# Kernel optimization log

Hardware: AMD Instinct MI355X
Metric: run time of the kernel (lower is better)

## Reference

```python
import jax, jax.numpy as jnp
import numpy as np

IN_F = 256
OUT_F = 256
ALPHA = 0.2  # LeakyReLU negative slope
NEG_INF = -9e15


def setup_inputs() -> dict:
    key = jax.random.key(0)
    k_h, k_adj, k_w, k_a = jax.random.split(key, 4)
    N = 8192
    h = jax.random.normal(k_h, (N, IN_F), dtype=jnp.float32)
    adj = jax.random.randint(k_adj, (N, N), 0, 2, dtype=jnp.int32)
    # xavier_uniform with gain=1.414
    gain = 1.414
    limW = gain * np.sqrt(6.0 / (IN_F + OUT_F))
    W = jax.random.uniform(k_w, (IN_F, OUT_F), minval=-limW, maxval=limW, dtype=jnp.float32)
    lima = gain * np.sqrt(6.0 / (2 * OUT_F + 1))
    a = jax.random.uniform(k_a, (2 * OUT_F, 1), minval=-lima, maxval=lima, dtype=jnp.float32)
    return {"h": h, "adj": adj, "W": W, "a": a}


def reference(h, adj, W, a):
    # Wh: [N, F]
    Wh = h @ W
    # The original materializes [N, N, 2F] concat pairs; equivalently
    # e[i, j] = leakyrelu(Wh[i] . a[:F] + Wh[j] . a[F:])
    a1 = a[:OUT_F, 0]  # [F]
    a2 = a[OUT_F:, 0]  # [F]
    s1 = Wh @ a1       # [N]
    s2 = Wh @ a2       # [N]
    e = jax.nn.leaky_relu(s1[:, None] + s2[None, :], negative_slope=ALPHA)  # [N, N]
    att = jnp.where(adj > 0, e, NEG_INF)
    att = jax.nn.softmax(att, axis=1)
    # dropout p=0.0 (eval) -> identity
    h_prime = att @ Wh  # [N, F]
    return jax.nn.elu(h_prime)  # concat=True path
```

## Files before the change

kernel.cpp:

```cpp
#include <hip/hip_runtime.h>

#define NN 8192
#define FF 256
#define PST 136

typedef _Float16 h8 __attribute__((ext_vector_type(8)));
typedef _Float16 h4 __attribute__((ext_vector_type(4)));
typedef float    f4 __attribute__((ext_vector_type(4)));
typedef int      i4v __attribute__((ext_vector_type(4)));

__device__ __forceinline__ unsigned fenc(float x) {
  unsigned u = __float_as_uint(x);
  return (u & 0x80000000u) ? ~u : (u | 0x80000000u);
}
__device__ __forceinline__ float fdec(unsigned e) {
  unsigned u = (e & 0x80000000u) ? (e ^ 0x80000000u) : ~e;
  return __uint_as_float(u);
}

__device__ __forceinline__ void sync_lds() {
  __builtin_amdgcn_s_waitcnt(0xc07f);
  __builtin_amdgcn_s_barrier();
}

__global__ __launch_bounds__(256) void k_wh(
    const float* __restrict__ h, const float* __restrict__ W,
    const float* __restrict__ a, _Float16* __restrict__ wfrag,
    float* __restrict__ s1, _Float16* __restrict__ s2h,
    unsigned* __restrict__ s2maxe) {
  __shared__ float hs[16 * 256];
  __shared__ _Float16 whs[16 * 264];
  const int t = threadIdx.x;
  const int r0 = blockIdx.x * 16;
#pragma unroll
  for (int i = 0; i < 4; ++i) {
    int idx = i * 1024 + t * 4;
    *(f4*)&hs[idx] = *(const f4*)&h[(size_t)r0 * 256 + idx];
  }
  __syncthreads();
  const int lane = t & 63;
  const int wv = t >> 6;
  const int rg = wv * 4;
  const int c4 = lane * 4;
  float acc[4][4];
#pragma unroll
  for (int i = 0; i < 4; ++i)
#pragma unroll
    for (int k = 0; k < 4; ++k) acc[i][k] = 0.f;
  f4 w[8];
#pragma unroll
  for (int i = 0; i < 8; ++i) w[i] = *(const f4*)&W[i * 256 + c4];
  for (int f = 0; f < 256; f += 8) {
    f4 nw[8];
    if (f < 248) {
#pragma unroll
      for (int i = 0; i < 8; ++i) nw[i] = *(const f4*)&W[(f + 8 + i) * 256 + c4];
    }
#pragma unroll
    for (int i = 0; i < 4; ++i) {
      f4 h0 = *(const f4*)&hs[(rg + i) * 256 + f];
      f4 h1 = *(const f4*)&hs[(rg + i) * 256 + f + 4];
#pragma unroll
      for (int k = 0; k < 4; ++k)
        acc[i][k] += h0[0]*w[0][k] + h0[1]*w[1][k] + h0[2]*w[2][k] + h0[3]*w[3][k]
                   + h1[0]*w[4][k] + h1[1]*w[5][k] + h1[2]*w[6][k] + h1[3]*w[7][k];
    }
    if (f < 248) {
#pragma unroll
      for (int i = 0; i < 8; ++i) w[i] = nw[i];
    }
  }
  float a1v[4], a2v[4];
#pragma unroll
  for (int k = 0; k < 4; ++k) { a1v[k] = a[c4 + k]; a2v[k] = a[256 + c4 + k]; }
#pragma unroll
  for (int i = 0; i < 4; ++i) {
    h4 hh;
    float p1 = 0.f, p2 = 0.f;
#pragma unroll
    for (int k = 0; k < 4; ++k) {
      hh[k] = (_Float16)acc[i][k];
      p1 += acc[i][k] * a1v[k];
      p2 += acc[i][k] * a2v[k];
    }
    *(h4*)&whs[(rg + i) * 264 + c4] = hh;
#pragma unroll
    for (int off = 32; off; off >>= 1) {
      p1 += __shfl_xor(p1, off);
      p2 += __shfl_xor(p2, off);
    }
    if (lane == 0) {
      const int r = r0 + rg + i;
      s1[r] = p1;
      s2h[r] = (_Float16)p2;
      atomicMax(s2maxe, fenc(p2));
    }
  }
  __syncthreads();
  {
    const int kt = blockIdx.x >> 1;
    const int hb = blockIdx.x & 1;
    const int lp = hb * 32 + (t & 31);
    const int kb = ((t & 31) >> 4) * 8;
    const int m16e = t & 15;
#pragma unroll
    for (int p = 0; p < 2; ++p) {
      const int n = (t >> 5) + p * 8;
      h8 v;
#pragma unroll
      for (int j = 0; j < 8; ++j) v[j] = whs[(kb + j) * 264 + n * 16 + m16e];
      *(h8*)&wfrag[(((size_t)kt * 16 + n) << 9) + lp * 8] = v;
    }
  }
}

__global__ __launch_bounds__(512, 4) void k_gat(
    const int* __restrict__ adj, const _Float16* __restrict__ wfrag,
    const float* __restrict__ s1g, const _Float16* __restrict__ s2h,
    const unsigned* __restrict__ s2maxe,
    float* __restrict__ o0, float* __restrict__ o1,
    float* __restrict__ lbuf) {
  __shared__ _Float16 P[2][32 * PST];
  __shared__ _Float16 s2l[4096];
  const int t = threadIdx.x;
  const int lane = t & 63;
  const int w = t >> 6;
  const int q = lane >> 4;
  const int m16 = lane & 15;
  const int rt = (int)blockIdx.x >> 1;
  const int kh = (int)blockIdx.x & 1;
  const int r0 = rt * 32;

  ((h8*)s2l)[t] = ((const h8*)(s2h + kh * 4096))[t];

  const int srow = 4 * w + q;
  const float s2m = fdec(*s2maxe);
  const float s1r = s1g[r0 + srow];
  const float u0 = s1r + s2m;
  const float mi = fmaxf(u0, 0.2f * u0);
  const float s1mi = s1r - mi;

  f4 acc[2][2];
#pragma unroll
  for (int m = 0; m < 2; ++m)
#pragma unroll
    for (int n = 0; n < 2; ++n)
#pragma unroll
      for (int e = 0; e < 4; ++e) acc[m][n][e] = 0.f;
  float lsum = 0.f;

  const int* adjp = adj + (size_t)(r0 + srow) * NN + kh * 4096 + m16 * 8;
  __syncthreads();

  i4v c0 = *(const i4v*)(adjp);
  i4v c1 = *(const i4v*)(adjp + 4);

  for (int p = 0; p < 32; ++p) {
    const _Float16* wfb =
        wfrag + ((((size_t)(kh * 128 + p * 4)) * 16 + 2 * w) << 9) + lane * 8;
    h8 bb[8];
#pragma unroll
    for (int ks = 0; ks < 4; ++ks) {
      bb[2 * ks]     = *(const h8*)(wfb + ks * 8192);
      bb[2 * ks + 1] = *(const h8*)(wfb + ks * 8192 + 512);
    }
    i4v n0 = c0, n1 = c1;
    if (p < 31) {
      n0 = *(const i4v*)(adjp + (p + 1) * 128);
      n1 = *(const i4v*)(adjp + (p + 1) * 128 + 4);
    }
    const h8 s2c = *(const h8*)&s2l[p * 128 + m16 * 8];
    h8 pa;
#pragma unroll
    for (int j = 0; j < 8; ++j) {
      const float s2v = (float)s2c[j];
      const float u = s1r + s2v;
      const float arg = s1mi + s2v - 0.8f * fminf(u, 0.f);
      const int msk = (j < 4) ? c0[j] : c1[j - 4];
      const float pv = (msk > 0) ? __expf(arg) : 0.f;
      lsum += pv;
      pa[j] = (_Float16)pv;
    }
    _Float16* Pb = &P[p & 1][0];
    *(h8*)&Pb[srow * PST + m16 * 8] = pa;
    sync_lds();
#pragma unroll
    for (int ks = 0; ks < 4; ++ks) {
      const h8 A0 = *(const h8*)&Pb[m16 * PST + ks * 32 + q * 8];
      const h8 A1 = *(const h8*)&Pb[(16 + m16) * PST + ks * 32 + q * 8];
      acc[0][0] = __builtin_amdgcn_mfma_f32_16x16x32_f16(A0, bb[2*ks],   acc[0][0], 0, 0, 0);
      acc[0][1] = __builtin_amdgcn_mfma_f32_16x16x32_f16(A0, bb[2*ks+1], acc[0][1], 0, 0, 0);
      acc[1][0] = __builtin_amdgcn_mfma_f32_16x16x32_f16(A1, bb[2*ks],   acc[1][0], 0, 0, 0);
      acc[1][1] = __builtin_amdgcn_mfma_f32_16x16x32_f16(A1, bb[2*ks+1], acc[1][1], 0, 0, 0);
    }
    c0 = n0; c1 = n1;
  }

  lsum += __shfl_xor(lsum, 1);
  lsum += __shfl_xor(lsum, 2);
  lsum += __shfl_xor(lsum, 4);
  lsum += __shfl_xor(lsum, 8);
  if (m16 == 0) lbuf[kh * NN + r0 + srow] = lsum;

  float* ob = kh ? o1 : o0;
#pragma unroll
  for (int m = 0; m < 2; ++m)
#pragma unroll
    for (int n = 0; n < 2; ++n)
#pragma unroll
      for (int v = 0; v < 4; ++v)
        ob[(size_t)(r0 + m * 16 + q * 4 + v) * FF + w * 32 + n * 16 + m16] =
            acc[m][n][v];
}

__global__ __launch_bounds__(256) void k_fin(
    float* __restrict__ out, const float* __restrict__ o1,
    const float* __restrict__ lbuf) {
  const int t = threadIdx.x;
  const int row = blockIdx.x * 16 + (t >> 4);
  const int c0 = (t & 15) * 16;
  const float linv = 1.0f / (lbuf[row] + lbuf[NN + row]);
#pragma unroll
  for (int i = 0; i < 4; ++i) {
    f4 v0 = *(const f4*)&out[(size_t)row * FF + c0 + i * 4];
    f4 v1 = *(const f4*)&o1[(size_t)row * FF + c0 + i * 4];
    f4 o;
#pragma unroll
    for (int e = 0; e < 4; ++e) {
      float x = (v0[e] + v1[e]) * linv;
      o[e] = (x > 0.f) ? x : (__expf(x) - 1.f);
    }
    *(f4*)&out[(size_t)row * FF + c0 + i * 4] = o;
  }
}

extern "C" void kernel_launch(void* const* d_in, const int* in_sizes, int n_in,
                              void* d_out, int out_size, void* d_ws, size_t ws_size,
                              hipStream_t stream) {
  const float* h   = (const float*)d_in[0];
  const int*   adj = (const int*)d_in[1];
  const float* W   = (const float*)d_in[2];
  const float* a   = (const float*)d_in[3];
  float* out = (float*)d_out;

  char* ws = (char*)d_ws;
  _Float16* wfrag = (_Float16*)ws;
  float*    o1    = (float*)(ws + (4u << 20));
  float*    lbuf  = (float*)(ws + (12u << 20));
  unsigned* s2me  = (unsigned*)(ws + (12u << 20) + 65536);
  float*    s1    = (float*)(ws + (12u << 20) + 65600);
  _Float16* s2h   = (_Float16*)(ws + (12u << 20) + 65600 + 32768);

  hipMemsetAsync(s2me, 0, 4, stream);
  k_wh<<<512, 256, 0, stream>>>(h, W, a, wfrag, s1, s2h, s2me);
  k_gat<<<512, 512, 0, stream>>>(adj, wfrag, s1, s2h, s2me, out, o1, lbuf);
  k_fin<<<512, 256, 0, stream>>>(out, o1, lbuf);
}
```

Baseline: 502.7 us.

## Prefetch adjacency into bitmask upfront and double-buffer wfrag B fragments

```diff
diff --git a/kernel.cpp b/kernel.cpp
--- a/kernel.cpp
+++ b/kernel.cpp
@@ -140,6 +140,26 @@
   const float mi = fmaxf(u0, 0.2f * u0);
   const float s1mi = s1r - mi;
 
+  const int* adjp = adj + (size_t)(r0 + srow) * NN + kh * 4096 + m16 * 8;
+  unsigned bits[8] = {0, 0, 0, 0, 0, 0, 0, 0};
+  {
+    i4v buf[16];
+#pragma unroll
+    for (int i = 0; i < 16; ++i)
+      buf[i] = __builtin_nontemporal_load(
+          (const i4v*)(adjp + (i >> 1) * 128 + (i & 1) * 4));
+#pragma unroll
+    for (int i = 0; i < 64; ++i) {
+      const i4v v = buf[i & 15];
+      if (i + 16 < 64)
+        buf[i & 15] = __builtin_nontemporal_load(
+            (const i4v*)(adjp + ((i + 16) >> 1) * 128 + ((i + 16) & 1) * 4));
+      const unsigned nib = (unsigned)(v[0] > 0) | ((unsigned)(v[1] > 0) << 1) |
+                           ((unsigned)(v[2] > 0) << 2) | ((unsigned)(v[3] > 0) << 3);
+      bits[i >> 3] |= nib << ((((i >> 1) & 3) << 3) + ((i & 1) << 2));
+    }
+  }
+
   f4 acc[2][2];
 #pragma unroll
   for (int m = 0; m < 2; ++m)
@@ -149,26 +169,30 @@
       for (int e = 0; e < 4; ++e) acc[m][n][e] = 0.f;
   float lsum = 0.f;
 
-  const int* adjp = adj + (size_t)(r0 + srow) * NN + kh * 4096 + m16 * 8;
   __syncthreads();
 
-  i4v c0 = *(const i4v*)(adjp);
-  i4v c1 = *(const i4v*)(adjp + 4);
-
-  for (int p = 0; p < 32; ++p) {
+  h8 bb[2][8];
+  {
     const _Float16* wfb =
-        wfrag + ((((size_t)(kh * 128 + p * 4)) * 16 + 2 * w) << 9) + lane * 8;
-    h8 bb[8];
+        wfrag + ((((size_t)(kh * 128)) * 16 + 2 * w) << 9) + lane * 8;
 #pragma unroll
     for (int ks = 0; ks < 4; ++ks) {
-      bb[2 * ks]     = *(const h8*)(wfb + ks * 8192);
-      bb[2 * ks + 1] = *(const h8*)(wfb + ks * 8192 + 512);
-    }
-    i4v n0 = c0, n1 = c1;
+      bb[0][2 * ks]     = *(const h8*)(wfb + ks * 8192);
+      bb[0][2 * ks + 1] = *(const h8*)(wfb + ks * 8192 + 512);
+    }
+  }
+
+  auto period = [&](int p, h8 (&bcur)[8], h8 (&bnxt)[8]) {
     if (p < 31) {
-      n0 = *(const i4v*)(adjp + (p + 1) * 128);
-      n1 = *(const i4v*)(adjp + (p + 1) * 128 + 4);
-    }
+      const _Float16* wfn =
+          wfrag + ((((size_t)(kh * 128 + (p + 1) * 4)) * 16 + 2 * w) << 9) + lane * 8;
+#pragma unroll
+      for (int ks = 0; ks < 4; ++ks) {
+        bnxt[2 * ks]     = *(const h8*)(wfn + ks * 8192);
+        bnxt[2 * ks + 1] = *(const h8*)(wfn + ks * 8192 + 512);
+      }
+    }
+    const unsigned byte = (bits[p >> 2] >> ((p & 3) << 3)) & 0xffu;
     const h8 s2c = *(const h8*)&s2l[p * 128 + m16 * 8];
     h8 pa;
 #pragma unroll
@@ -176,8 +200,7 @@
       const float s2v = (float)s2c[j];
       const float u = s1r + s2v;
       const float arg = s1mi + s2v - 0.8f * fminf(u, 0.f);
-      const int msk = (j < 4) ? c0[j] : c1[j - 4];
-      const float pv = (msk > 0) ? __expf(arg) : 0.f;
+      const float pv = (byte & (1u << j)) ? __expf(arg) : 0.f;
       lsum += pv;
       pa[j] = (_Float16)pv;
     }
@@ -188,12 +211,16 @@
     for (int ks = 0; ks < 4; ++ks) {
       const h8 A0 = *(const h8*)&Pb[m16 * PST + ks * 32 + q * 8];
       const h8 A1 = *(const h8*)&Pb[(16 + m16) * PST + ks * 32 + q * 8];
-      acc[0][0] = __builtin_amdgcn_mfma_f32_16x16x32_f16(A0, bb[2*ks],   acc[0][0], 0, 0, 0);
-      acc[0][1] = __builtin_amdgcn_mfma_f32_16x16x32_f16(A0, bb[2*ks+1], acc[0][1], 0, 0, 0);
-      acc[1][0] = __builtin_amdgcn_mfma_f32_16x16x32_f16(A1, bb[2*ks],   acc[1][0], 0, 0, 0);
-      acc[1][1] = __builtin_amdgcn_mfma_f32_16x16x32_f16(A1, bb[2*ks+1], acc[1][1], 0, 0, 0);
-    }
-    c0 = n0; c1 = n1;
+      acc[0][0] = __builtin_amdgcn_mfma_f32_16x16x32_f16(A0, bcur[2*ks],   acc[0][0], 0, 0, 0);
+      acc[0][1] = __builtin_amdgcn_mfma_f32_16x16x32_f16(A0, bcur[2*ks+1], acc[0][1], 0, 0, 0);
+      acc[1][0] = __builtin_amdgcn_mfma_f32_16x16x32_f16(A1, bcur[2*ks],   acc[1][0], 0, 0, 0);
+      acc[1][1] = __builtin_amdgcn_mfma_f32_16x16x32_f16(A1, bcur[2*ks+1], acc[1][1], 0, 0, 0);
+    }
+  };
+
+  for (int pp = 0; pp < 16; ++pp) {
+    period(2 * pp,     bb[0], bb[1]);
+    period(2 * pp + 1, bb[1], bb[0]);
   }
 
   lsum += __shfl_xor(lsum, 1);
```

Measured after the change: 537.5 us. 6.9% more time.

## Enlarge GAT row tile to 128 rows and split columns four ways

Applied to the files above, without the earlier changes.

```diff
diff --git a/kernel.cpp b/kernel.cpp
--- a/kernel.cpp
+++ b/kernel.cpp
@@ -114,123 +114,142 @@
   }
 }
 
-__global__ __launch_bounds__(512, 4) void k_gat(
+__global__ __launch_bounds__(512, 2) void k_gat(
     const int* __restrict__ adj, const _Float16* __restrict__ wfrag,
     const float* __restrict__ s1g, const _Float16* __restrict__ s2h,
     const unsigned* __restrict__ s2maxe,
     float* __restrict__ o0, float* __restrict__ o1,
+    float* __restrict__ o2, float* __restrict__ o3,
     float* __restrict__ lbuf) {
-  __shared__ _Float16 P[2][32 * PST];
-  __shared__ _Float16 s2l[4096];
+  __shared__ _Float16 P[2][128 * PST];
+  __shared__ _Float16 s2l[2048];
   const int t = threadIdx.x;
   const int lane = t & 63;
   const int w = t >> 6;
   const int q = lane >> 4;
   const int m16 = lane & 15;
-  const int rt = (int)blockIdx.x >> 1;
-  const int kh = (int)blockIdx.x & 1;
-  const int r0 = rt * 32;
-
-  ((h8*)s2l)[t] = ((const h8*)(s2h + kh * 4096))[t];
-
-  const int srow = 4 * w + q;
+  const int rt = (int)blockIdx.x >> 2;
+  const int kq = (int)blockIdx.x & 3;
+  const int r0 = rt * 128;
+
+  if (t < 256) ((h8*)s2l)[t] = ((const h8*)(s2h + kq * 2048))[t];
+
+  const int rloc = w * 16 + m16;
   const float s2m = fdec(*s2maxe);
-  const float s1r = s1g[r0 + srow];
+  const float s1r = s1g[r0 + rloc];
   const float u0 = s1r + s2m;
   const float mi = fmaxf(u0, 0.2f * u0);
   const float s1mi = s1r - mi;
 
-  f4 acc[2][2];
-#pragma unroll
-  for (int m = 0; m < 2; ++m)
+  f4 acc[8][2];
+#pragma unroll
+  for (int mt = 0; mt < 8; ++mt)
 #pragma unroll
     for (int n = 0; n < 2; ++n)
 #pragma unroll
-      for (int e = 0; e < 4; ++e) acc[m][n][e] = 0.f;
+      for (int e = 0; e < 4; ++e) acc[mt][n][e] = 0.f;
   float lsum = 0.f;
 
-  const int* adjp = adj + (size_t)(r0 + srow) * NN + kh * 4096 + m16 * 8;
+  const int* adjp = adj + (size_t)(r0 + rloc) * NN + kq * 2048 + q * 8;
   __syncthreads();
 
-  i4v c0 = *(const i4v*)(adjp);
-  i4v c1 = *(const i4v*)(adjp + 4);
-
-  for (int p = 0; p < 32; ++p) {
-    const _Float16* wfb =
-        wfrag + ((((size_t)(kh * 128 + p * 4)) * 16 + 2 * w) << 9) + lane * 8;
+  i4v adjc[8], adjn[8];
+#pragma unroll
+  for (int ks = 0; ks < 4; ++ks) {
+    adjc[2 * ks]     = __builtin_nontemporal_load((const i4v*)(adjp + ks * 32));
+    adjc[2 * ks + 1] = __builtin_nontemporal_load((const i4v*)(adjp + ks * 32 + 4));
+  }
+
+  for (int p = 0; p < 16; ++p) {
+    const int kb = kq * 64 + p * 4;
     h8 bb[8];
 #pragma unroll
     for (int ks = 0; ks < 4; ++ks) {
-      bb[2 * ks]     = *(const h8*)(wfb + ks * 8192);
-      bb[2 * ks + 1] = *(const h8*)(wfb + ks * 8192 + 512);
-    }
-    i4v n0 = c0, n1 = c1;
-    if (p < 31) {
-      n0 = *(const i4v*)(adjp + (p + 1) * 128);
-      n1 = *(const i4v*)(adjp + (p + 1) * 128 + 4);
-    }
-    const h8 s2c = *(const h8*)&s2l[p * 128 + m16 * 8];
-    h8 pa;
-#pragma unroll
-    for (int j = 0; j < 8; ++j) {
-      const float s2v = (float)s2c[j];
-      const float u = s1r + s2v;
-      const float arg = s1mi + s2v - 0.8f * fminf(u, 0.f);
-      const int msk = (j < 4) ? c0[j] : c1[j - 4];
-      const float pv = (msk > 0) ? __expf(arg) : 0.f;
-      lsum += pv;
-      pa[j] = (_Float16)pv;
+      const _Float16* wfb =
+          wfrag + (((size_t)(kb + ks) * 16 + 2 * w) << 9) + lane * 8;
+      bb[2 * ks]     = *(const h8*)(wfb);
+      bb[2 * ks + 1] = *(const h8*)(wfb + 512);
+    }
+    if (p < 15) {
+#pragma unroll
+      for (int ks = 0; ks < 4; ++ks) {
+        adjn[2 * ks]     = __builtin_nontemporal_load(
+            (const i4v*)(adjp + (p + 1) * 128 + ks * 32));
+        adjn[2 * ks + 1] = __builtin_nontemporal_load(
+            (const i4v*)(adjp + (p + 1) * 128 + ks * 32 + 4));
+      }
     }
     _Float16* Pb = &P[p & 1][0];
-    *(h8*)&Pb[srow * PST + m16 * 8] = pa;
+#pragma unroll
+    for (int ks = 0; ks < 4; ++ks) {
+      const h8 s2c = *(const h8*)&s2l[p * 128 + ks * 32 + q * 8];
+      const i4v a0 = adjc[2 * ks];
+      const i4v a1 = adjc[2 * ks + 1];
+      h8 pa;
+#pragma unroll
+      for (int j = 0; j < 8; ++j) {
+        const float s2v = (float)s2c[j];
+        const float u = s1r + s2v;
+        const float arg = s1mi + s2v - 0.8f * fminf(u, 0.f);
+        const int msk = (j < 4) ? a0[j] : a1[j - 4];
+        const float pv = (msk > 0) ? __expf(arg) : 0.f;
+        lsum += pv;
+        pa[j] = (_Float16)pv;
+      }
+      *(h8*)&Pb[rloc * PST + ks * 32 + q * 8] = pa;
+    }
     sync_lds();
 #pragma unroll
     for (int ks = 0; ks < 4; ++ks) {
-      const h8 A0 = *(const h8*)&Pb[m16 * PST + ks * 32 + q * 8];
-      const h8 A1 = *(const h8*)&Pb[(16 + m16) * PST + ks * 32 + q * 8];
-      acc[0][0] = __builtin_amdgcn_mfma_f32_16x16x32_f16(A0, bb[2*ks],   acc[0][0], 0, 0, 0);
-      acc[0][1] = __builtin_amdgcn_mfma_f32_16x16x32_f16(A0, bb[2*ks+1], acc[0][1], 0, 0, 0);
-      acc[1][0] = __builtin_amdgcn_mfma_f32_16x16x32_f16(A1, bb[2*ks],   acc[1][0], 0, 0, 0);
-      acc[1][1] = __builtin_amdgcn_mfma_f32_16x16x32_f16(A1, bb[2*ks+1], acc[1][1], 0, 0, 0);
-    }
-    c0 = n0; c1 = n1;
-  }
-
-  lsum += __shfl_xor(lsum, 1);
-  lsum += __shfl_xor(lsum, 2);
-  lsum += __shfl_xor(lsum, 4);
-  lsum += __shfl_xor(lsum, 8);
-  if (m16 == 0) lbuf[kh * NN + r0 + srow] = lsum;
-
-  float* ob = kh ? o1 : o0;
-#pragma unroll
-  for (int m = 0; m < 2; ++m)
+#pragma unroll
+      for (int mt = 0; mt < 8; ++mt) {
+        const h8 A = *(const h8*)&Pb[(mt * 16 + m16) * PST + ks * 32 + q * 8];
+        acc[mt][0] = __builtin_amdgcn_mfma_f32_16x16x32_f16(A, bb[2*ks],   acc[mt][0], 0, 0, 0);
+        acc[mt][1] = __builtin_amdgcn_mfma_f32_16x16x32_f16(A, bb[2*ks+1], acc[mt][1], 0, 0, 0);
+      }
+    }
+#pragma unroll
+    for (int i = 0; i < 8; ++i) adjc[i] = adjn[i];
+  }
+
+  lsum += __shfl_xor(lsum, 16);
+  lsum += __shfl_xor(lsum, 32);
+  if (q == 0) lbuf[kq * NN + r0 + rloc] = lsum;
+
+  float* ob = (kq == 0) ? o0 : (kq == 1) ? o1 : (kq == 2) ? o2 : o3;
+#pragma unroll
+  for (int mt = 0; mt < 8; ++mt)
 #pragma unroll
     for (int n = 0; n < 2; ++n)
 #pragma unroll
       for (int v = 0; v < 4; ++v)
-        ob[(size_t)(r0 + m * 16 + q * 4 + v) * FF + w * 32 + n * 16 + m16] =
-            acc[m][n][v];
+        ob[(size_t)(r0 + mt * 16 + q * 4 + v) * FF + w * 32 + n * 16 + m16] =
+            acc[mt][n][v];
 }
 
 __global__ __launch_bounds__(256) void k_fin(
     float* __restrict__ out, const float* __restrict__ o1,
+    const float* __restrict__ o2, const float* __restrict__ o3,
     const float* __restrict__ lbuf) {
   const int t = threadIdx.x;
   const int row = blockIdx.x * 16 + (t >> 4);
   const int c0 = (t & 15) * 16;
-  const float linv = 1.0f / (lbuf[row] + lbuf[NN + row]);
+  const float linv = 1.0f / (lbuf[row] + lbuf[NN + row] +
+                             lbuf[2 * NN + row] + lbuf[3 * NN + row]);
 #pragma unroll
   for (int i = 0; i < 4; ++i) {
-    f4 v0 = *(const f4*)&out[(size_t)row * FF + c0 + i * 4];
-    f4 v1 = *(const f4*)&o1[(size_t)row * FF + c0 + i * 4];
+    const size_t off = (size_t)row * FF + c0 + i * 4;
+    f4 v0 = *(const f4*)&out[off];
+    f4 v1 = *(const f4*)&o1[off];
+    f4 v2 = *(const f4*)&o2[off];
+    f4 v3 = *(const f4*)&o3[off];
     f4 o;
 #pragma unroll
     for (int e = 0; e < 4; ++e) {
-      float x = (v0[e] + v1[e]) * linv;
+      float x = (v0[e] + v1[e] + v2[e] + v3[e]) * linv;
       o[e] = (x > 0.f) ? x : (__expf(x) - 1.f);
     }
-    *(f4*)&out[(size_t)row * FF + c0 + i * 4] = o;
+    *(f4*)&out[off] = o;
   }
 }
 
@@ -246,13 +265,16 @@
   char* ws = (char*)d_ws;
   _Float16* wfrag = (_Float16*)ws;
   float*    o1    = (float*)(ws + (4u << 20));
-  float*    lbuf  = (float*)(ws + (12u << 20));
-  unsigned* s2me  = (unsigned*)(ws + (12u << 20) + 65536);
-  float*    s1    = (float*)(ws + (12u << 20) + 65600);
-  _Float16* s2h   = (_Float16*)(ws + (12u << 20) + 65600 + 32768);
+  float*    o2    = (float*)(ws + (12u << 20));
+  float*    o3    = (float*)(ws + (20u << 20));
+  float*    lbuf  = (float*)(ws + (28u << 20));
+  unsigned* s2me  = (unsigned*)(ws + (28u << 20) + 131072);
+  float*    s1    = (float*)(ws + (28u << 20) + 131136);
+  _Float16* s2h   = (_Float16*)(ws + (28u << 20) + 131136 + 32768);
 
   hipMemsetAsync(s2me, 0, 4, stream);
   k_wh<<<512, 256, 0, stream>>>(h, W, a, wfrag, s1, s2h, s2me);
-  k_gat<<<512, 512, 0, stream>>>(adj, wfrag, s1, s2h, s2me, out, o1, lbuf);
-  k_fin<<<512, 256, 0, stream>>>(out, o1, lbuf);
-}
+  k_gat<<<256, 512, 0, stream>>>(adj, wfrag, s1, s2h, s2me,
+                                 out, o1, o2, o3, lbuf);
+  k_fin<<<512, 256, 0, stream>>>(out, o1, o2, o3, lbuf);
+}
```

Result: slower. 514.9 us (+2.4%).
